# Optimization experiments

Measured on AMD Instinct MI355X. Metric: run time of the kernel, lower is better.

## Reference

```python
import jax, jax.numpy as jnp
import numpy as np

B, N, D, K = 32, 4096, 256, 16
EPS = 1e-12  # F.normalize default eps


def setup_inputs() -> dict:
    key = jax.random.key(0)
    k1, k2, k3, k4, k5 = jax.random.split(key, 5)
    x = jax.random.normal(k1, (B, N, D), dtype=jnp.float32)
    mask = jax.random.randint(k2, (B, N), 0, 2).astype(bool)
    W = jax.random.normal(k3, (K, D), dtype=jnp.float32) * 0.02
    b = jax.random.normal(k4, (K,), dtype=jnp.float32) * 0.02
    centroids = jax.random.normal(k5, (K, D), dtype=jnp.float32) * 0.02
    return {"x": x, "mask": mask, "W": W, "b": b, "centroids": centroids}


def reference(x, mask, W, b, centroids):
    # logits: (B, N, K); masked tokens get -1e9 on every cluster
    logits = jnp.einsum('bnd,kd->bnk', x, W) + b
    logits = jnp.where(mask[..., None], logits, jnp.float32(-1e9))
    assign = jax.nn.softmax(logits, axis=-1) * mask[..., None].astype(x.dtype)
    # vlad[b,k,:] = sum_n assign[b,n,k] * (x[b,n,:] - c[k,:])
    #            = (assign^T @ x) - (sum_n assign) * c   (avoids (B,N,K,D) tensor)
    vlad = jnp.einsum('bnk,bnd->bkd', assign, x) \
           - jnp.sum(assign, axis=1)[..., None] * centroids[None]
    # intra-cluster L2 normalize (dim=2)
    vlad = vlad / jnp.maximum(jnp.linalg.norm(vlad, axis=2, keepdims=True), EPS)
    vlad = vlad.reshape(x.shape[0], K * D)
    # global L2 normalize (dim=1)
    return vlad / jnp.maximum(jnp.linalg.norm(vlad, axis=1, keepdims=True), EPS)
```

## Files before the change

kernel.cpp:

```cpp
#include <hip/hip_runtime.h>
#include <cstdint>
#include <cstddef>

#define BB 32
#define NN 4096
#define DD 256
#define KK 16

constexpr float FEPS = 1e-12f;

__device__ __forceinline__ float dot4(float4 a, float4 b) {
  return a.x*b.x + a.y*b.y + a.z*b.z + a.w*b.w;
}
__device__ __forceinline__ float4 f4add(float4 a, float4 b) {
  return make_float4(a.x+b.x, a.y+b.y, a.z+b.z, a.w+b.w);
}

template <int TILE>
__global__ __launch_bounds__(256, (TILE == 64 ? 8 : 4)) void fused_kernel(
    const float* __restrict__ x, const int* __restrict__ mask,
    const float* __restrict__ W, const float* __restrict__ bias,
    float* __restrict__ outv, float* __restrict__ outs, int partial_mode)
{
  constexpr int NG    = 256 / TILE;
  constexpr int KPT   = KK / NG;
  constexpr int SW4   = TILE / 64;
  constexpr int WPG   = 4 / NG;
  constexpr int TPBAT = NN / TILE;

  __shared__ float4 xs4[2][TILE * 5];
  __shared__ float  al[TILE][KK];
  __shared__ float  psum[TILE][NG];
  __shared__ float  asacc[WPG][KK];

  const int tid  = threadIdx.x;
  const int lane = tid & 63;
  const int wave = tid >> 6;
  const int tok  = tid & (TILE - 1);
  const int kg   = __builtin_amdgcn_readfirstlane(tid / TILE);
  const int slot = __builtin_amdgcn_readfirstlane(wave & (WPG - 1));

  const int tile = blockIdx.x;
  const int b    = tile / TPBAT;
  const int n0   = (tile % TPBAT) * TILE;

  const float4* xb4 = reinterpret_cast<const float4*>(x + ((size_t)b*NN + n0)*DD);
  const int*    mb  = mask + (size_t)b*NN + n0;

  float part[KPT];
#pragma unroll
  for (int q = 0; q < KPT; ++q) part[q] = bias[kg * KPT + q];

  const int st = tid >> 2;
  const int sj = tid & 3;

  {
    float4 pre[SW4];
#pragma unroll
    for (int l = 0; l < SW4; ++l)
      pre[l] = xb4[(size_t)(st + l * 64) * 64 + sj];
#pragma unroll
    for (int l = 0; l < SW4; ++l)
      xs4[0][(st + l * 64) * 5 + sj] = pre[l];
  }

#pragma unroll 1
  for (int c = 0; c < 16; ++c) {
    __syncthreads();
    const int cur = c & 1;

    float4 nxt[SW4];
    if (c < 15) {
#pragma unroll
      for (int l = 0; l < SW4; ++l)
        nxt[l] = xb4[(size_t)(st + l * 64) * 64 + (c + 1) * 4 + sj];
    }

#pragma unroll
    for (int j = 0; j < 4; ++j) {
      const float4 xv = xs4[cur][tok * 5 + j];
      const float* Wc = W + c * 16 + j * 4;
#pragma unroll
      for (int q = 0; q < KPT; ++q) {
        const float4 wv = *reinterpret_cast<const float4*>(Wc + (kg * KPT + q) * DD);
        part[q] += dot4(xv, wv);
      }
    }

    if (c < 15) {
#pragma unroll
      for (int l = 0; l < SW4; ++l)
        xs4[cur ^ 1][(st + l * 64) * 5 + sj] = nxt[l];
    }
  }

  float e[KPT], pexp = 0.f;
#pragma unroll
  for (int q = 0; q < KPT; ++q) { e[q] = __expf(part[q]); pexp += e[q]; }
  psum[tok][kg] = pexp;
  __syncthreads();
  float a[KPT];
  {
    float denom = 0.f;
#pragma unroll
    for (int g = 0; g < NG; ++g) denom += psum[tok][g];
    const float r = mb[tok] ? (1.0f / denom) : 0.0f;
#pragma unroll
    for (int q = 0; q < KPT; ++q) a[q] = e[q] * r;
#pragma unroll
    for (int q4 = 0; q4 < KPT; q4 += 4)
      *reinterpret_cast<float4*>(&al[tok][kg * KPT + q4]) =
          make_float4(a[q4], a[q4+1], a[q4+2], a[q4+3]);
  }

  {
    float red[KPT];
#pragma unroll
    for (int q = 0; q < KPT; ++q) red[q] = a[q];
#pragma unroll
    for (int off = 32; off >= 1; off >>= 1)
#pragma unroll
      for (int q = 0; q < KPT; ++q) red[q] += __shfl_xor(red[q], off);
    if (lane == 0)
#pragma unroll
      for (int q = 0; q < KPT; ++q) asacc[slot][kg * KPT + q] = red[q];
  }
  __syncthreads();

  float4 acc0 = make_float4(0.f,0.f,0.f,0.f);
  float4 acc1 = make_float4(0.f,0.f,0.f,0.f);
  float4 acc2 = make_float4(0.f,0.f,0.f,0.f);
  float4 acc3 = make_float4(0.f,0.f,0.f,0.f);

  const float4* xw = xb4 + lane;
  const int kq = wave * 4;

#pragma unroll 4
  for (int t = 0; t < TILE; ++t) {
    const float4 xv = xw[(size_t)t * 64];
    const float4 av = *reinterpret_cast<const float4*>(&al[t][kq]);
    acc0.x += av.x*xv.x; acc0.y += av.x*xv.y; acc0.z += av.x*xv.z; acc0.w += av.x*xv.w;
    acc1.x += av.y*xv.x; acc1.y += av.y*xv.y; acc1.z += av.y*xv.z; acc1.w += av.y*xv.w;
    acc2.x += av.z*xv.x; acc2.y += av.z*xv.y; acc2.z += av.z*xv.z; acc2.w += av.z*xv.w;
    acc3.x += av.w*xv.x; acc3.y += av.w*xv.y; acc3.z += av.w*xv.z; acc3.w += av.w*xv.w;
  }

  if (partial_mode) {
    float4* dst = reinterpret_cast<float4*>(outv + (size_t)tile * KK * DD);
    dst[(kq + 0) * 64 + lane] = acc0;
    dst[(kq + 1) * 64 + lane] = acc1;
    dst[(kq + 2) * 64 + lane] = acc2;
    dst[(kq + 3) * 64 + lane] = acc3;
    if (tid < KK) {
      float s = 0.f;
#pragma unroll
      for (int sl = 0; sl < WPG; ++sl) s += asacc[sl][tid];
      outs[tile * KK + tid] = s;
    }
  } else {
    float* vb = outv + (size_t)b * KK * DD;
    const float4 aa[4] = {acc0, acc1, acc2, acc3};
#pragma unroll
    for (int i = 0; i < 4; ++i) {
      float* p = vb + (kq + i) * DD + 4 * lane;
      atomicAdd(p + 0, aa[i].x);
      atomicAdd(p + 1, aa[i].y);
      atomicAdd(p + 2, aa[i].z);
      atomicAdd(p + 3, aa[i].w);
    }
    if (tid < KK) {
      float s = 0.f;
#pragma unroll
      for (int sl = 0; sl < WPG; ++sl) s += asacc[sl][tid];
      atomicAdd(&outs[b * KK + tid], s);
    }
  }
}

__global__ __launch_bounds__(256) void finalizeA_kernel(
    const float* __restrict__ pv, const float* __restrict__ ps,
    const float* __restrict__ cent, float* __restrict__ vtmp,
    float* __restrict__ ssbuf, int nslice)
{
  const int blk = blockIdx.x;
  const int b   = blk >> 4;
  const int k   = blk & 15;
  const int tid = threadIdx.x;
  const int sg  = tid >> 6;
  const int ld  = tid & 63;

  __shared__ float4 cmbA[3][64];

  float pval = 0.f;
  for (int s = ld; s < nslice; s += 64)
    pval += ps[(size_t)(b * nslice + s) * KK + k];
#pragma unroll
  for (int off = 32; off >= 1; off >>= 1) pval += __shfl_xor(pval, off);
  const float ssum = pval;

  const float4* pv4 = reinterpret_cast<const float4*>(pv);
  const size_t base = ((size_t)b * nslice * KK + k) * 64 + ld;
  float4 a0 = make_float4(0.f,0.f,0.f,0.f), a1 = a0, a2 = a0, a3 = a0;
  int s = sg;
  for (; s + 12 < nslice; s += 16) {
    a0 = f4add(a0, pv4[base + (size_t)(s     ) * (KK * 64)]);
    a1 = f4add(a1, pv4[base + (size_t)(s +  4) * (KK * 64)]);
    a2 = f4add(a2, pv4[base + (size_t)(s +  8) * (KK * 64)]);
    a3 = f4add(a3, pv4[base + (size_t)(s + 12) * (KK * 64)]);
  }
  for (; s < nslice; s += 4)
    a0 = f4add(a0, pv4[base + (size_t)s * (KK * 64)]);
  float4 tot = f4add(f4add(a0, a1), f4add(a2, a3));

  if (sg > 0) cmbA[sg - 1][ld] = tot;
  __syncthreads();

  if (sg == 0) {
    tot = f4add(tot, f4add(cmbA[0][ld], f4add(cmbA[1][ld], cmbA[2][ld])));
    const float4 cv = reinterpret_cast<const float4*>(cent)[k * 64 + ld];
    float4 v;
    v.x = tot.x - ssum * cv.x;
    v.y = tot.y - ssum * cv.y;
    v.z = tot.z - ssum * cv.z;
    v.w = tot.w - ssum * cv.w;
    reinterpret_cast<float4*>(vtmp)[((size_t)b * KK + k) * 64 + ld] = v;
    float p = dot4(v, v);
#pragma unroll
    for (int off = 32; off >= 1; off >>= 1) p += __shfl_xor(p, off);
    if (ld == 0) ssbuf[blk] = p;
  }
}

__global__ __launch_bounds__(1024) void finalizeB_kernel(
    const float* __restrict__ vtmp, const float* __restrict__ ssbuf,
    float* __restrict__ out)
{
  const int b    = blockIdx.x;
  const int tid  = threadIdx.x;
  const int d    = tid & 255;
  const int kq   = tid >> 8;
  const int lane = tid & 63;
  const int w    = tid >> 6;

  __shared__ float redB[16];
  __shared__ float gsh;

  float u[4];
  float p2 = 0.f;
#pragma unroll
  for (int kk = 0; kk < 4; ++kk) {
    const int k = kq * 4 + kk;
    const float rk = 1.0f / fmaxf(sqrtf(ssbuf[b * KK + k]), FEPS);
    u[kk] = vtmp[((size_t)b * KK + k) * DD + d] * rk;
    p2 += u[kk] * u[kk];
  }
#pragma unroll
  for (int off = 32; off >= 1; off >>= 1) p2 += __shfl_xor(p2, off);
  if (lane == 0) redB[w] = p2;
  __syncthreads();

  if (tid == 0) {
    float g = 0.f;
#pragma unroll
    for (int i = 0; i < 16; ++i) g += redB[i];
    gsh = 1.0f / fmaxf(sqrtf(g), FEPS);
  }
  __syncthreads();

  const float g = gsh;
#pragma unroll
  for (int kk = 0; kk < 4; ++kk) {
    const int k = kq * 4 + kk;
    out[(size_t)b * KK * DD + k * DD + d] = u[kk] * g;
  }
}

extern "C" void kernel_launch(void* const* d_in, const int* in_sizes, int n_in,
                              void* d_out, int out_size, void* d_ws, size_t ws_size,
                              hipStream_t stream) {
  const float* x    = (const float*)d_in[0];
  const int*   mask = (const int*)d_in[1];
  const float* W    = (const float*)d_in[2];
  const float* bias = (const float*)d_in[3];
  const float* cent = (const float*)d_in[4];
  float* out = (float*)d_out;

  const size_t vtmpN = (size_t)BB * KK * DD;
  const size_t ssN   = (size_t)BB * KK;

  const size_t t64   = (size_t)BB * (NN / 64);
  const size_t t128  = (size_t)BB * (NN / 128);
  const size_t need64  = (t64  * KK * DD + t64  * KK + vtmpN + ssN) * sizeof(float);
  const size_t need128 = (t128 * KK * DD + t128 * KK + vtmpN + ssN) * sizeof(float);

  if (ws_size >= need64) {
    float* pv    = (float*)d_ws;
    float* ps    = pv + t64 * KK * DD;
    float* vtmp  = ps + t64 * KK;
    float* ssbuf = vtmp + vtmpN;
    fused_kernel<64><<<(int)t64, 256, 0, stream>>>(x, mask, W, bias, pv, ps, 1);
    finalizeA_kernel<<<BB * KK, 256, 0, stream>>>(pv, ps, cent, vtmp, ssbuf, NN / 64);
    finalizeB_kernel<<<BB, 1024, 0, stream>>>(vtmp, ssbuf, out);
  } else if (ws_size >= need128) {
    float* pv    = (float*)d_ws;
    float* ps    = pv + t128 * KK * DD;
    float* vtmp  = ps + t128 * KK;
    float* ssbuf = vtmp + vtmpN;
    fused_kernel<128><<<(int)t128, 256, 0, stream>>>(x, mask, W, bias, pv, ps, 1);
    finalizeA_kernel<<<BB * KK, 256, 0, stream>>>(pv, ps, cent, vtmp, ssbuf, NN / 128);
    finalizeB_kernel<<<BB, 1024, 0, stream>>>(vtmp, ssbuf, out);
  } else {
    float* vacc  = (float*)d_ws;
    float* sacc  = vacc + vtmpN;
    float* vtmp  = sacc + ssN;
    float* ssbuf = vtmp + vtmpN;
    hipMemsetAsync(d_ws, 0, (vtmpN + ssN) * sizeof(float), stream);
    fused_kernel<64><<<(int)t64, 256, 0, stream>>>(x, mask, W, bias, vacc, sacc, 0);
    finalizeA_kernel<<<BB * KK, 256, 0, stream>>>(vacc, sacc, cent, vtmp, ssbuf, 1);
    finalizeB_kernel<<<BB, 1024, 0, stream>>>(vtmp, ssbuf, out);
  }
}
```

Measured before the change: 63.57 us.

## Restructure fused kernel into 16-token sub-tiles with full rows staged in LDS

```diff
diff --git a/kernel.cpp b/kernel.cpp
--- a/kernel.cpp
+++ b/kernel.cpp
@@ -7,6 +7,12 @@
 #define DD 256
 #define KK 16
 
+constexpr int TILE  = 64;
+constexpr int SUB   = 16;
+constexpr int NSUB  = TILE / SUB;
+constexpr int TPBAT = NN / TILE;
+constexpr int TILES = BB * TPBAT;
+constexpr int ROWF  = 260;
 constexpr float FEPS = 1e-12f;
 
 __device__ __forceinline__ float dot4(float4 a, float4 b) {
@@ -16,29 +22,20 @@
   return make_float4(a.x+b.x, a.y+b.y, a.z+b.z, a.w+b.w);
 }
 
-template <int TILE>
-__global__ __launch_bounds__(256, (TILE == 64 ? 8 : 4)) void fused_kernel(
+__global__ __launch_bounds__(256, 8) void fused_kernel(
     const float* __restrict__ x, const int* __restrict__ mask,
     const float* __restrict__ W, const float* __restrict__ bias,
     float* __restrict__ outv, float* __restrict__ outs, int partial_mode)
 {
-  constexpr int NG    = 256 / TILE;
-  constexpr int KPT   = KK / NG;
-  constexpr int SW4   = TILE / 64;
-  constexpr int WPG   = 4 / NG;
-  constexpr int TPBAT = NN / TILE;
-
-  __shared__ float4 xs4[2][TILE * 5];
-  __shared__ float  al[TILE][KK];
-  __shared__ float  psum[TILE][NG];
-  __shared__ float  asacc[WPG][KK];
+  __shared__ float xs[SUB * ROWF];
+  __shared__ float al[SUB * KK];
 
   const int tid  = threadIdx.x;
   const int lane = tid & 63;
   const int wave = tid >> 6;
-  const int tok  = tid & (TILE - 1);
-  const int kg   = __builtin_amdgcn_readfirstlane(tid / TILE);
-  const int slot = __builtin_amdgcn_readfirstlane(wave & (WPG - 1));
+  const int tp   = tid >> 5;
+  const int dc   = (tid >> 4) & 1;
+  const int k    = tid & 15;
 
   const int tile = blockIdx.x;
   const int b    = tile / TPBAT;
@@ -47,132 +44,111 @@
   const float4* xb4 = reinterpret_cast<const float4*>(x + ((size_t)b*NN + n0)*DD);
   const int*    mb  = mask + (size_t)b*NN + n0;
 
-  float part[KPT];
-#pragma unroll
-  for (int q = 0; q < KPT; ++q) part[q] = bias[kg * KPT + q];
-
-  const int st = tid >> 2;
-  const int sj = tid & 3;
+  const float  bk = bias[k];
+  const float* Wh = W + k * DD + dc * 128;
+
+  float4 acc0 = make_float4(0.f,0.f,0.f,0.f);
+  float4 acc1 = acc0, acc2 = acc0, acc3 = acc0, asum = acc0;
 
   {
-    float4 pre[SW4];
-#pragma unroll
-    for (int l = 0; l < SW4; ++l)
-      pre[l] = xb4[(size_t)(st + l * 64) * 64 + sj];
-#pragma unroll
-    for (int l = 0; l < SW4; ++l)
-      xs4[0][(st + l * 64) * 5 + sj] = pre[l];
-  }
-
-#pragma unroll 1
-  for (int c = 0; c < 16; ++c) {
+    float4 s0 = xb4[0*256 + tid], s1 = xb4[1*256 + tid],
+           s2 = xb4[2*256 + tid], s3 = xb4[3*256 + tid];
+    int i;
+    i = 0*256 + tid; *reinterpret_cast<float4*>(xs + (i>>6)*ROWF + (i&63)*4) = s0;
+    i = 1*256 + tid; *reinterpret_cast<float4*>(xs + (i>>6)*ROWF + (i&63)*4) = s1;
+    i = 2*256 + tid; *reinterpret_cast<float4*>(xs + (i>>6)*ROWF + (i&63)*4) = s2;
+    i = 3*256 + tid; *reinterpret_cast<float4*>(xs + (i>>6)*ROWF + (i&63)*4) = s3;
+  }
+
+#pragma unroll
+  for (int st = 0; st < NSUB; ++st) {
     __syncthreads();
-    const int cur = c & 1;
-
-    float4 nxt[SW4];
-    if (c < 15) {
-#pragma unroll
-      for (int l = 0; l < SW4; ++l)
-        nxt[l] = xb4[(size_t)(st + l * 64) * 64 + (c + 1) * 4 + sj];
-    }
-
-#pragma unroll
-    for (int j = 0; j < 4; ++j) {
-      const float4 xv = xs4[cur][tok * 5 + j];
-      const float* Wc = W + c * 16 + j * 4;
-#pragma unroll
-      for (int q = 0; q < KPT; ++q) {
-        const float4 wv = *reinterpret_cast<const float4*>(Wc + (kg * KPT + q) * DD);
-        part[q] += dot4(xv, wv);
-      }
-    }
-
-    if (c < 15) {
-#pragma unroll
-      for (int l = 0; l < SW4; ++l)
-        xs4[cur ^ 1][(st + l * 64) * 5 + sj] = nxt[l];
-    }
-  }
-
-  float e[KPT], pexp = 0.f;
-#pragma unroll
-  for (int q = 0; q < KPT; ++q) { e[q] = __expf(part[q]); pexp += e[q]; }
-  psum[tok][kg] = pexp;
-  __syncthreads();
-  float a[KPT];
-  {
-    float denom = 0.f;
-#pragma unroll
-    for (int g = 0; g < NG; ++g) denom += psum[tok][g];
-    const float r = mb[tok] ? (1.0f / denom) : 0.0f;
-#pragma unroll
-    for (int q = 0; q < KPT; ++q) a[q] = e[q] * r;
-#pragma unroll
-    for (int q4 = 0; q4 < KPT; q4 += 4)
-      *reinterpret_cast<float4*>(&al[tok][kg * KPT + q4]) =
-          make_float4(a[q4], a[q4+1], a[q4+2], a[q4+3]);
-  }
-
-  {
-    float red[KPT];
-#pragma unroll
-    for (int q = 0; q < KPT; ++q) red[q] = a[q];
-#pragma unroll
-    for (int off = 32; off >= 1; off >>= 1)
-#pragma unroll
-      for (int q = 0; q < KPT; ++q) red[q] += __shfl_xor(red[q], off);
-    if (lane == 0)
-#pragma unroll
-      for (int q = 0; q < KPT; ++q) asacc[slot][kg * KPT + q] = red[q];
-  }
-  __syncthreads();
-
-  float4 acc0 = make_float4(0.f,0.f,0.f,0.f);
-  float4 acc1 = make_float4(0.f,0.f,0.f,0.f);
-  float4 acc2 = make_float4(0.f,0.f,0.f,0.f);
-  float4 acc3 = make_float4(0.f,0.f,0.f,0.f);
-
-  const float4* xw = xb4 + lane;
+
+    float4 n0v, n1v, n2v, n3v;
+    if (st < NSUB - 1) {
+      const int o = (st + 1) * (SUB * 64);
+      n0v = xb4[o + 0*256 + tid]; n1v = xb4[o + 1*256 + tid];
+      n2v = xb4[o + 2*256 + tid]; n3v = xb4[o + 3*256 + tid];
+    }
+    const int mva = mb[st*SUB + 2*tp + 0];
+    const int mvb = mb[st*SUB + 2*tp + 1];
+
+    const float* rowA = xs + (2*tp + 0) * ROWF + dc * 128;
+    const float* rowB = xs + (2*tp + 1) * ROWF + dc * 128;
+    float pa0 = 0.f, pa1 = 0.f, pb0 = 0.f, pb1 = 0.f;
+#pragma unroll 2
+    for (int j = 0; j < 32; ++j) {
+      const float4 wv  = *reinterpret_cast<const float4*>(Wh   + j*4);
+      const float4 xva = *reinterpret_cast<const float4*>(rowA + j*4);
+      const float4 xvb = *reinterpret_cast<const float4*>(rowB + j*4);
+      if (j & 1) { pa1 += dot4(xva, wv); pb1 += dot4(xvb, wv); }
+      else       { pa0 += dot4(xva, wv); pb0 += dot4(xvb, wv); }
+    }
+    float la = pa0 + pa1, lb = pb0 + pb1;
+    la += __shfl_xor(la, 16);
+    lb += __shfl_xor(lb, 16);
+    la += bk; lb += bk;
+
+    float ea = __expf(la), eb = __expf(lb);
+    float sa = ea, sb = eb;
+    sa += __shfl_xor(sa, 1); sb += __shfl_xor(sb, 1);
+    sa += __shfl_xor(sa, 2); sb += __shfl_xor(sb, 2);
+    sa += __shfl_xor(sa, 4); sb += __shfl_xor(sb, 4);
+    sa += __shfl_xor(sa, 8); sb += __shfl_xor(sb, 8);
+    const float aa = mva ? ea / sa : 0.0f;
+    const float ab = mvb ? eb / sb : 0.0f;
+    if (dc == 0) {
+      al[(2*tp + 0) * KK + k] = aa;
+      al[(2*tp + 1) * KK + k] = ab;
+    }
+    __syncthreads();
+
+#pragma unroll 4
+    for (int t = 0; t < SUB; ++t) {
+      const float4 av = *reinterpret_cast<const float4*>(al + t*KK + 4*wave);
+      const float4 xv = *reinterpret_cast<const float4*>(xs + t*ROWF + 4*lane);
+      acc0.x += av.x*xv.x; acc0.y += av.x*xv.y; acc0.z += av.x*xv.z; acc0.w += av.x*xv.w;
+      acc1.x += av.y*xv.x; acc1.y += av.y*xv.y; acc1.z += av.y*xv.z; acc1.w += av.y*xv.w;
+      acc2.x += av.z*xv.x; acc2.y += av.z*xv.y; acc2.z += av.z*xv.z; acc2.w += av.z*xv.w;
+      acc3.x += av.w*xv.x; acc3.y += av.w*xv.y; acc3.z += av.w*xv.z; acc3.w += av.w*xv.w;
+      asum = f4add(asum, av);
+    }
+
+    if (st < NSUB - 1) {
+      __syncthreads();
+      int i;
+      i = 0*256 + tid; *reinterpret_cast<float4*>(xs + (i>>6)*ROWF + (i&63)*4) = n0v;
+      i = 1*256 + tid; *reinterpret_cast<float4*>(xs + (i>>6)*ROWF + (i&63)*4) = n1v;
+      i = 2*256 + tid; *reinterpret_cast<float4*>(xs + (i>>6)*ROWF + (i&63)*4) = n2v;
+      i = 3*256 + tid; *reinterpret_cast<float4*>(xs + (i>>6)*ROWF + (i&63)*4) = n3v;
+    }
+  }
+
   const int kq = wave * 4;
-
-#pragma unroll 4
-  for (int t = 0; t < TILE; ++t) {
-    const float4 xv = xw[(size_t)t * 64];
-    const float4 av = *reinterpret_cast<const float4*>(&al[t][kq]);
-    acc0.x += av.x*xv.x; acc0.y += av.x*xv.y; acc0.z += av.x*xv.z; acc0.w += av.x*xv.w;
-    acc1.x += av.y*xv.x; acc1.y += av.y*xv.y; acc1.z += av.y*xv.z; acc1.w += av.y*xv.w;
-    acc2.x += av.z*xv.x; acc2.y += av.z*xv.y; acc2.z += av.z*xv.z; acc2.w += av.z*xv.w;
-    acc3.x += av.w*xv.x; acc3.y += av.w*xv.y; acc3.z += av.w*xv.z; acc3.w += av.w*xv.w;
-  }
-
   if (partial_mode) {
     float4* dst = reinterpret_cast<float4*>(outv + (size_t)tile * KK * DD);
     dst[(kq + 0) * 64 + lane] = acc0;
     dst[(kq + 1) * 64 + lane] = acc1;
     dst[(kq + 2) * 64 + lane] = acc2;
     dst[(kq + 3) * 64 + lane] = acc3;
-    if (tid < KK) {
-      float s = 0.f;
-#pragma unroll
-      for (int sl = 0; sl < WPG; ++sl) s += asacc[sl][tid];
-      outs[tile * KK + tid] = s;
-    }
+    if (lane == 0)
+      *reinterpret_cast<float4*>(outs + tile * KK + kq) = asum;
   } else {
     float* vb = outv + (size_t)b * KK * DD;
-    const float4 aa[4] = {acc0, acc1, acc2, acc3};
+    const float4 aa4[4] = {acc0, acc1, acc2, acc3};
 #pragma unroll
     for (int i = 0; i < 4; ++i) {
       float* p = vb + (kq + i) * DD + 4 * lane;
-      atomicAdd(p + 0, aa[i].x);
-      atomicAdd(p + 1, aa[i].y);
-      atomicAdd(p + 2, aa[i].z);
-      atomicAdd(p + 3, aa[i].w);
-    }
-    if (tid < KK) {
-      float s = 0.f;
-#pragma unroll
-      for (int sl = 0; sl < WPG; ++sl) s += asacc[sl][tid];
-      atomicAdd(&outs[b * KK + tid], s);
+      atomicAdd(p + 0, aa4[i].x);
+      atomicAdd(p + 1, aa4[i].y);
+      atomicAdd(p + 2, aa4[i].z);
+      atomicAdd(p + 3, aa4[i].w);
+    }
+    if (lane == 0) {
+      atomicAdd(&outs[b * KK + kq + 0], asum.x);
+      atomicAdd(&outs[b * KK + kq + 1], asum.y);
+      atomicAdd(&outs[b * KK + kq + 2], asum.z);
+      atomicAdd(&outs[b * KK + kq + 3], asum.w);
     }
   }
 }
@@ -287,27 +263,16 @@
 
   const size_t vtmpN = (size_t)BB * KK * DD;
   const size_t ssN   = (size_t)BB * KK;
-
-  const size_t t64   = (size_t)BB * (NN / 64);
-  const size_t t128  = (size_t)BB * (NN / 128);
-  const size_t need64  = (t64  * KK * DD + t64  * KK + vtmpN + ssN) * sizeof(float);
-  const size_t need128 = (t128 * KK * DD + t128 * KK + vtmpN + ssN) * sizeof(float);
-
-  if (ws_size >= need64) {
+  const size_t need  = ((size_t)TILES * KK * DD + (size_t)TILES * KK
+                        + vtmpN + ssN) * sizeof(float);
+
+  if (ws_size >= need) {
     float* pv    = (float*)d_ws;
-    float* ps    = pv + t64 * KK * DD;
-    float* vtmp  = ps + t64 * KK;
+    float* ps    = pv + (size_t)TILES * KK * DD;
+    float* vtmp  = ps + (size_t)TILES * KK;
     float* ssbuf = vtmp + vtmpN;
-    fused_kernel<64><<<(int)t64, 256, 0, stream>>>(x, mask, W, bias, pv, ps, 1);
-    finalizeA_kernel<<<BB * KK, 256, 0, stream>>>(pv, ps, cent, vtmp, ssbuf, NN / 64);
-    finalizeB_kernel<<<BB, 1024, 0, stream>>>(vtmp, ssbuf, out);
-  } else if (ws_size >= need128) {
-    float* pv    = (float*)d_ws;
-    float* ps    = pv + t128 * KK * DD;
-    float* vtmp  = ps + t128 * KK;
-    float* ssbuf = vtmp + vtmpN;
-    fused_kernel<128><<<(int)t128, 256, 0, stream>>>(x, mask, W, bias, pv, ps, 1);
-    finalizeA_kernel<<<BB * KK, 256, 0, stream>>>(pv, ps, cent, vtmp, ssbuf, NN / 128);
+    fused_kernel<<<TILES, 256, 0, stream>>>(x, mask, W, bias, pv, ps, 1);
+    finalizeA_kernel<<<BB * KK, 256, 0, stream>>>(pv, ps, cent, vtmp, ssbuf, TPBAT);
     finalizeB_kernel<<<BB, 1024, 0, stream>>>(vtmp, ssbuf, out);
   } else {
     float* vacc  = (float*)d_ws;
@@ -315,7 +280,7 @@
     float* vtmp  = sacc + ssN;
     float* ssbuf = vtmp + vtmpN;
     hipMemsetAsync(d_ws, 0, (vtmpN + ssN) * sizeof(float), stream);
-    fused_kernel<64><<<(int)t64, 256, 0, stream>>>(x, mask, W, bias, vacc, sacc, 0);
+    fused_kernel<<<TILES, 256, 0, stream>>>(x, mask, W, bias, vacc, sacc, 0);
     finalizeA_kernel<<<BB * KK, 256, 0, stream>>>(vacc, sacc, cent, vtmp, ssbuf, 1);
     finalizeB_kernel<<<BB, 1024, 0, stream>>>(vtmp, ssbuf, out);
   }
```

Measured after the change: 164.8 us. 2.59x slower.
